# Kernel tuning notes

Hardware: AMD Instinct MI355X
Metric: run time of the kernel (lower is better)

## Reference

```python
import jax, jax.numpy as jnp
import numpy as np

EMBED = 1024
HEADS = 16
HEAD_DIM = EMBED // HEADS
LN_EPS = 1e-5


def _layer_norm(x, g, b):
    m = jnp.mean(x, axis=-1, keepdims=True)
    v = jnp.mean((x - m) ** 2, axis=-1, keepdims=True)
    return (x - m) / jnp.sqrt(v + LN_EPS) * g + b


def _rope(x):
    # x: (b, H, n, D); standard rotary: freqs repeated (cat(freqs, freqs)), rotate_half
    D = x.shape[-1]
    n = x.shape[2]
    inv_freq = 1.0 / (10000.0 ** (jnp.arange(0, D, 2, dtype=jnp.float32) / D))
    freqs = jnp.arange(n, dtype=jnp.float32)[:, None] * inv_freq[None, :]  # (n, D/2)
    emb = jnp.concatenate([freqs, freqs], axis=-1)  # (n, D)
    cos, sin = jnp.cos(emb), jnp.sin(emb)
    rot = jnp.concatenate([-x[..., D // 2:], x[..., : D // 2]], axis=-1)
    return x * cos + rot * sin


def setup_inputs() -> dict:
    key = jax.random.key(0)
    ks = jax.random.split(key, 8)
    E = EMBED
    s_in = 1.0 / np.sqrt(E)
    return {
        "x": jax.random.normal(ks[0], (2, 2048, E), dtype=jnp.float32),
        "in_proj_w": jax.random.uniform(ks[1], (3 * E, E), jnp.float32, -s_in, s_in),
        "in_proj_b": jnp.zeros((3 * E,), jnp.float32),
        "out_proj_w": jax.random.uniform(ks[2], (E, E), jnp.float32, -s_in, s_in),
        "out_proj_b": jnp.zeros((E,), jnp.float32),
        "geglu_w": jax.random.uniform(ks[3], (2 * E, E), jnp.float32, -s_in, s_in),
        "geglu_b": jnp.zeros((2 * E,), jnp.float32),
        "ln1_g": jnp.ones((E,), jnp.float32),
        "ln1_b": jnp.zeros((E,), jnp.float32),
        "ln2_g": jnp.ones((E,), jnp.float32),
        "ln2_b": jnp.zeros((E,), jnp.float32),
    }


def reference(x, in_proj_w, in_proj_b, out_proj_w, out_proj_b,
              geglu_w, geglu_b, ln1_g, ln1_b, ln2_g, ln2_b):
    b, n, E = x.shape
    H, D = HEADS, HEAD_DIM

    # RoPE applied to raw x (q = k = v = x in the module)
    xh = x.reshape(b, n, H, D).transpose(0, 2, 1, 3)  # (b,H,n,D)
    qr = _rope(xh)
    kr = qr  # q and k are identical pre-projection
    q = qr.transpose(0, 2, 1, 3).reshape(b, n, E)
    k = kr.transpose(0, 2, 1, 3).reshape(b, n, E)
    v = x

    # MultiheadAttention (batch-first semantics): in-proj, per-head SDPA, out-proj
    w_q, w_k, w_v = jnp.split(in_proj_w, 3, axis=0)
    b_q, b_k, b_v = jnp.split(in_proj_b, 3, axis=0)
    qp = (q @ w_q.T + b_q).reshape(b, n, H, D).transpose(0, 2, 1, 3)
    kp = (k @ w_k.T + b_k).reshape(b, n, H, D).transpose(0, 2, 1, 3)
    vp = (v @ w_v.T + b_v).reshape(b, n, H, D).transpose(0, 2, 1, 3)
    scores = jnp.einsum("bhqd,bhkd->bhqk", qp, kp) / jnp.sqrt(jnp.float32(D))
    attn = jax.nn.softmax(scores, axis=-1)
    ctx = jnp.einsum("bhqk,bhkd->bhqd", attn, vp)
    ctx = ctx.transpose(0, 2, 1, 3).reshape(b, n, E)
    attn_out = ctx @ out_proj_w.T + out_proj_b

    # residual + LN1
    h = _layer_norm(x + attn_out, ln1_g, ln1_b)

    # GeGLU: Linear(E -> 2E), chunk, value * gelu(gate) (exact erf gelu like torch)
    proj = h @ geglu_w.T + geglu_b
    val, gate = jnp.split(proj, 2, axis=-1)
    fc_out = val * jax.nn.gelu(gate, approximate=False)

    # residual + LN2
    return _layer_norm(h + fc_out, ln2_g, ln2_b)
```

## Files before the change

kernel.cpp:

```cpp
#include <hip/hip_runtime.h>


typedef __bf16 bf16;
typedef bf16 bf16x8 __attribute__((ext_vector_type(8)));
typedef bf16 bf16x4 __attribute__((ext_vector_type(4)));
typedef float f32x4 __attribute__((ext_vector_type(4)));
typedef float f32x16 __attribute__((ext_vector_type(16)));

#define EMB 1024
#define SEQ 2048
#define NTOK 4096
#define NH 16
#define HD 64

__device__ __forceinline__ f32x4 mfma16(bf16x8 a, bf16x8 b, f32x4 c) {
  return __builtin_amdgcn_mfma_f32_16x16x32_bf16(a, b, c, 0, 0, 0);
}
__device__ __forceinline__ f32x16 mfma32(bf16x8 a, bf16x8 b, f32x16 c) {
  return __builtin_amdgcn_mfma_f32_32x32x16_bf16(a, b, c, 0, 0, 0);
}

__device__ __forceinline__ void gll16(const void* g, void* l) {
  __builtin_amdgcn_global_load_lds(
      (const __attribute__((address_space(1))) void*)g,
      (__attribute__((address_space(3))) void*)l, 16, 0, 0);
}

__device__ __forceinline__ unsigned pk2(float a, float b) {
  union { bf16 h[2]; unsigned u; } t;
  t.h[0] = (bf16)a; t.h[1] = (bf16)b;
  return t.u;
}


__global__ __launch_bounds__(256) void rope_cast(
    const float* __restrict__ x, bf16* __restrict__ xb, bf16* __restrict__ qr) {
  int idx = blockIdx.x * 256 + threadIdx.x;
  int row = idx >> 9;
  int i = idx & 511;
  int h = i >> 5, d2 = i & 31;
  int pos = row & (SEQ - 1);
  int c0 = h * HD + d2;
  size_t base = (size_t)row * EMB;
  float x0 = x[base + c0], x1 = x[base + c0 + 32];
  float invf = exp2f(-(float)d2 * 0.4152410118609203f);
  float ang = (float)pos * invf;
  float sn, cs;
  sincosf(ang, &sn, &cs);
  qr[base + c0] = (bf16)(x0 * cs - x1 * sn);
  qr[base + c0 + 32] = (bf16)(x1 * cs + x0 * sn);
  xb[base + c0] = (bf16)x0;
  xb[base + c0 + 32] = (bf16)x1;
}

__global__ __launch_bounds__(256) void cast_w(
    const float* __restrict__ w, bf16* __restrict__ o, int n) {
  int i = (blockIdx.x * 256 + threadIdx.x) * 4;
  if (i < n) {
    float4 f = *(const float4*)(w + i);
    o[i] = (bf16)f.x; o[i + 1] = (bf16)f.y;
    o[i + 2] = (bf16)f.z; o[i + 3] = (bf16)f.w;
  }
}

__global__ __launch_bounds__(256) void gemm_in(
    const bf16* __restrict__ Aq, const bf16* __restrict__ Ax,
    const bf16* __restrict__ W, const float* __restrict__ bias,
    bf16* __restrict__ qk, bf16* __restrict__ vT) {
  __shared__ bf16 As[128 * 32];
  __shared__ bf16 Bs[128 * 32];
  const int tid = threadIdx.x, lane = tid & 63, wave = tid >> 6;
  const int quad = lane >> 4, l16 = lane & 15;
  const int m0 = blockIdx.y * 128, n0 = blockIdx.x * 128;
  const bf16* A = (n0 < 2048) ? Aq : Ax;
  const int K = 1024;
  const int wm = (wave >> 1) * 64, wn = (wave & 1) * 64;
  const int srow = wave * 32 + (lane >> 2);
  const int scol = (lane & 3) * 8;
  f32x4 acc[4][4] = {};
  for (int k0 = 0; k0 < K; k0 += 32) {
    __syncthreads();
    gll16(A + (size_t)(m0 + srow) * K + k0 + scol, As + wave * 1024);
    gll16(A + (size_t)(m0 + srow + 16) * K + k0 + scol, As + wave * 1024 + 512);
    gll16(W + (size_t)(n0 + srow) * K + k0 + scol, Bs + wave * 1024);
    gll16(W + (size_t)(n0 + srow + 16) * K + k0 + scol, Bs + wave * 1024 + 512);
    __syncthreads();
    bf16x8 af[4], bw[4];
#pragma unroll
    for (int t = 0; t < 4; ++t) {
      af[t] = *(const bf16x8*)(As + (wm + t * 16 + l16) * 32 + quad * 8);
      bw[t] = *(const bf16x8*)(Bs + (wn + t * 16 + l16) * 32 + quad * 8);
    }
#pragma unroll
    for (int mt = 0; mt < 4; ++mt)
#pragma unroll
      for (int nt = 0; nt < 4; ++nt)
        acc[mt][nt] = mfma16(af[mt], bw[nt], acc[mt][nt]);
  }
  if (n0 < 2048) {
#pragma unroll
    for (int mt = 0; mt < 4; ++mt)
      for (int nt = 0; nt < 4; ++nt) {
        const int n = n0 + wn + nt * 16 + l16;
        const float bv = bias[n];
#pragma unroll
        for (int r = 0; r < 4; ++r) {
          const int m = m0 + wm + mt * 16 + quad * 4 + r;
          qk[(size_t)m * 2048 + n] = (bf16)(acc[mt][nt][r] + bv);
        }
      }
  } else {
#pragma unroll
    for (int mt = 0; mt < 4; ++mt)
      for (int nt = 0; nt < 4; ++nt) {
        const int n = n0 + wn + nt * 16 + l16;
        const float bv = bias[n];
        const int m = m0 + wm + mt * 16 + quad * 4;
        const int bb = m >> 11, s = m & 2047;
        bf16x4 pkv;
#pragma unroll
        for (int r = 0; r < 4; ++r) pkv[r] = (bf16)(acc[mt][nt][r] + bv);
        *(bf16x4*)(vT + (((size_t)bb * 1024 + (n - 2048)) << 11) + s) = pkv;
      }
  }
}

__global__ __launch_bounds__(256) void gemm_bt(
    const bf16* __restrict__ A, const bf16* __restrict__ W,
    const float* __restrict__ bias,
    float* __restrict__ outF, bf16* __restrict__ outB,
    int M, int N, int K) {
  __shared__ bf16 As[128 * 32];
  __shared__ bf16 Bs[128 * 32];
  const int tid = threadIdx.x, lane = tid & 63, wave = tid >> 6;
  const int quad = lane >> 4, l16 = lane & 15;
  const int m0 = blockIdx.y * 128, n0 = blockIdx.x * 128;
  const int wm = (wave >> 1) * 64, wn = (wave & 1) * 64;
  const int srow = wave * 32 + (lane >> 2);
  const int scol = (lane & 3) * 8;
  f32x4 acc[4][4] = {};
  for (int k0 = 0; k0 < K; k0 += 32) {
    __syncthreads();
    gll16(A + (size_t)(m0 + srow) * K + k0 + scol, As + wave * 1024);
    gll16(A + (size_t)(m0 + srow + 16) * K + k0 + scol, As + wave * 1024 + 512);
    gll16(W + (size_t)(n0 + srow) * K + k0 + scol, Bs + wave * 1024);
    gll16(W + (size_t)(n0 + srow + 16) * K + k0 + scol, Bs + wave * 1024 + 512);
    __syncthreads();
    bf16x8 af[4], bw[4];
#pragma unroll
    for (int t = 0; t < 4; ++t) {
      af[t] = *(const bf16x8*)(As + (wm + t * 16 + l16) * 32 + quad * 8);
      bw[t] = *(const bf16x8*)(Bs + (wn + t * 16 + l16) * 32 + quad * 8);
    }
#pragma unroll
    for (int mt = 0; mt < 4; ++mt)
#pragma unroll
      for (int nt = 0; nt < 4; ++nt)
        acc[mt][nt] = mfma16(af[mt], bw[nt], acc[mt][nt]);
  }
#pragma unroll
  for (int mt = 0; mt < 4; ++mt)
    for (int nt = 0; nt < 4; ++nt) {
      const int n = n0 + wn + nt * 16 + l16;
      const float bv = bias ? bias[n] : 0.0f;
#pragma unroll
      for (int r = 0; r < 4; ++r) {
        const int m = m0 + wm + mt * 16 + quad * 4 + r;
        const float v = acc[mt][nt][r] + bv;
        if (outF) outF[(size_t)m * N + n] = v;
        if (outB) outB[(size_t)m * N + n] = (bf16)v;
      }
    }
}

__global__ __launch_bounds__(256) void gemm_bt64(
    const bf16* __restrict__ A, const bf16* __restrict__ W,
    const float* __restrict__ bias, float* __restrict__ outF,
    int M, int N, int K) {
  __shared__ bf16 As[128 * 32];
  __shared__ bf16 Bs[64 * 32];
  const int tid = threadIdx.x, lane = tid & 63, wave = tid >> 6;
  const int quad = lane >> 4, l16 = lane & 15;
  const int m0 = blockIdx.y * 128, n0 = blockIdx.x * 64;
  const int wm = (wave >> 1) * 64, wn = (wave & 1) * 32;
  const int srow = wave * 32 + (lane >> 2);
  const int srowB = wave * 16 + (lane >> 2);
  const int scol = (lane & 3) * 8;
  f32x4 acc[4][2] = {};
  for (int k0 = 0; k0 < K; k0 += 32) {
    __syncthreads();
    gll16(A + (size_t)(m0 + srow) * K + k0 + scol, As + wave * 1024);
    gll16(A + (size_t)(m0 + srow + 16) * K + k0 + scol, As + wave * 1024 + 512);
    gll16(W + (size_t)(n0 + srowB) * K + k0 + scol, Bs + wave * 512);
    __syncthreads();
    bf16x8 af[4], bw[2];
#pragma unroll
    for (int t = 0; t < 4; ++t)
      af[t] = *(const bf16x8*)(As + (wm + t * 16 + l16) * 32 + quad * 8);
#pragma unroll
    for (int t = 0; t < 2; ++t)
      bw[t] = *(const bf16x8*)(Bs + (wn + t * 16 + l16) * 32 + quad * 8);
#pragma unroll
    for (int mt = 0; mt < 4; ++mt)
#pragma unroll
      for (int nt = 0; nt < 2; ++nt)
        acc[mt][nt] = mfma16(af[mt], bw[nt], acc[mt][nt]);
  }
#pragma unroll
  for (int mt = 0; mt < 4; ++mt)
    for (int nt = 0; nt < 2; ++nt) {
      const int n = n0 + wn + nt * 16 + l16;
      const float bv = bias[n];
#pragma unroll
      for (int r = 0; r < 4; ++r) {
        const int m = m0 + wm + mt * 16 + quad * 4 + r;
        outF[(size_t)m * N + n] = acc[mt][nt][r] + bv;
      }
    }
}

__global__ __launch_bounds__(256) void attn9(
    const bf16* __restrict__ QK, const bf16* __restrict__ VT,
    bf16* __restrict__ ctx) {
  __shared__ __align__(16) bf16 Ks[2][8192];
  __shared__ __align__(16) bf16 Vs[2][8192];
  __shared__ float Linv[4][32];
  const int tid = threadIdx.x, lane = tid & 63, wave = tid >> 6;
  const int hi = lane >> 5, l31 = lane & 31, l7 = lane & 7;
  const int bid = blockIdx.x;
  const int hb = (bid & 7) * 4 + ((bid >> 3) & 3);
  const int qt = bid >> 5;
  const int h = hb & 15, b = hb >> 4;

  bf16x8 qf[4];
  {
    const int qrow = qt * 128 + wave * 32 + l31;
    const bf16* qp = QK + (size_t)(b * SEQ + qrow) * 2048 + h * HD + hi * 8;
#pragma unroll
    for (int t = 0; t < 4; ++t) {
      bf16x8 v = *(const bf16x8*)(qp + t * 16);
#pragma unroll
      for (int j = 0; j < 8; ++j) v[j] = (bf16)((float)v[j] * 0.125f);
      qf[t] = v;
    }
  }
  f32x16 o0 = {}, o1 = {};
  float lpart = 0.0f;

  const int krow0 = tid >> 3;
  const int ksc = tid & 7;
  const int vrow0 = tid >> 4;
  const int vc16 = tid & 15;
  const int og = (vc16 >> 1) * 16 + (vc16 & 1) * 4;
  const bf16* kg = QK + (size_t)(b * SEQ) * 2048 + 1024 + h * HD + ksc * 8;
  const bf16* vg = VT + ((size_t)(b * NH + h) * HD) * 2048;

  bf16x8 kcur[4];
  uint2 va[4], vb[4];
#pragma unroll
  for (int p = 0; p < 4; ++p) {
    kcur[p] = *(const bf16x8*)(kg + (size_t)(krow0 + p * 32) * 2048);
    va[p] = *(const uint2*)(vg + (size_t)(vrow0 + p * 16) * 2048 + og);
    vb[p] = *(const uint2*)(vg + (size_t)(vrow0 + p * 16) * 2048 + og + 8);
  }
#pragma unroll
  for (int p = 0; p < 4; ++p) {
    const int kr = krow0 + p * 32;
    *(bf16x8*)(Ks[0] + kr * 64 + ((ksc ^ (kr & 7)) * 8)) = kcur[p];
    const int vr = vrow0 + p * 16;
    union { uint2 u2[2]; bf16x8 v; } vv;
    vv.u2[0] = va[p]; vv.u2[1] = vb[p];
    *(bf16x8*)(Vs[0] + vr * 128 + ((vc16 ^ (vr & 7)) * 8)) = vv.v;
  }
#pragma unroll
  for (int p = 0; p < 4; ++p) {
    kcur[p] = *(const bf16x8*)(kg + (size_t)(128 + krow0 + p * 32) * 2048);
    va[p] = *(const uint2*)(vg + (size_t)(vrow0 + p * 16) * 2048 + 128 + og);
    vb[p] = *(const uint2*)(vg + (size_t)(vrow0 + p * 16) * 2048 + 128 + og + 8);
  }

  for (int t = 0; t < 16; ++t) {
    __syncthreads();
    const bf16* ks = Ks[t & 1];
    const bf16* vs = Vs[t & 1];
    if (t + 1 < 16) {
      bf16* kd = Ks[(t + 1) & 1];
      bf16* vd = Vs[(t + 1) & 1];
#pragma unroll
      for (int p = 0; p < 4; ++p) {
        const int kr = krow0 + p * 32;
        *(bf16x8*)(kd + kr * 64 + ((ksc ^ (kr & 7)) * 8)) = kcur[p];
        const int vr = vrow0 + p * 16;
        union { uint2 u2[2]; bf16x8 v; } vv;
        vv.u2[0] = va[p]; vv.u2[1] = vb[p];
        *(bf16x8*)(vd + vr * 128 + ((vc16 ^ (vr & 7)) * 8)) = vv.v;
      }
      if (t + 2 < 16) {
        const int kb2 = (t + 2) * 128;
#pragma unroll
        for (int p = 0; p < 4; ++p) {
          kcur[p] = *(const bf16x8*)(kg + (size_t)(kb2 + krow0 + p * 32) * 2048);
          va[p] = *(const uint2*)(vg + (size_t)(vrow0 + p * 16) * 2048 + kb2 + og);
          vb[p] = *(const uint2*)(vg + (size_t)(vrow0 + p * 16) * 2048 + kb2 + og + 8);
        }
      }
    }
#pragma unroll
    for (int half = 0; half < 2; ++half) {
      const bf16* ksh = ks + half * 64 * 64;
      f32x16 s0 = {}, s1 = {};
#pragma unroll
      for (int tt = 0; tt < 4; ++tt) {
        const int swc = ((tt * 2 + hi) ^ l7) * 8;
        bf16x8 k0 = *(const bf16x8*)(ksh + l31 * 64 + swc);
        bf16x8 k1 = *(const bf16x8*)(ksh + (32 + l31) * 64 + swc);
        s0 = mfma32(k0, qf[tt], s0);
        s1 = mfma32(k1, qf[tt], s1);
      }
      unsigned u[16];
#pragma unroll
      for (int g = 0; g < 8; ++g) {
        const int base = (g & 3) * 4;
        float e0, e1, e2, e3;
        if (g < 4) {
          e0 = __expf(s0[base]); e1 = __expf(s0[base + 1]);
          e2 = __expf(s0[base + 2]); e3 = __expf(s0[base + 3]);
        } else {
          e0 = __expf(s1[base]); e1 = __expf(s1[base + 1]);
          e2 = __expf(s1[base + 2]); e3 = __expf(s1[base + 3]);
        }
        lpart += (e0 + e1) + (e2 + e3);
        u[g * 2] = pk2(e0, e1);
        u[g * 2 + 1] = pk2(e2, e3);
      }
#pragma unroll
      for (int kk = 0; kk < 4; ++kk) {
        union { unsigned w[4]; bf16x8 v; } fw;
        fw.w[0] = u[4 * kk]; fw.w[1] = u[4 * kk + 1];
        fw.w[2] = u[4 * kk + 2]; fw.w[3] = u[4 * kk + 3];
        const int c16 = (8 * half + 2 * kk + hi) ^ l7;
        bf16x8 v0 = *(const bf16x8*)(vs + l31 * 128 + c16 * 8);
        bf16x8 v1 = *(const bf16x8*)(vs + (32 + l31) * 128 + c16 * 8);
        o0 = mfma32(fw.v, v0, o0);
        o1 = mfma32(fw.v, v1, o1);
      }
    }
  }
  float ltot = lpart + __shfl_xor(lpart, 32, 64);
  if (lane < 32) Linv[wave][lane] = 1.0f / ltot;
#pragma unroll
  for (int r = 0; r < 16; ++r) {
    const int qloc = (r & 3) + 8 * (r >> 2) + 4 * hi;
    const float inv = Linv[wave][qloc];
    const int qrow = qt * 128 + wave * 32 + qloc;
    bf16* cp = ctx + (size_t)(b * SEQ + qrow) * EMB + h * HD;
    cp[l31] = (bf16)(o0[r] * inv);
    cp[32 + l31] = (bf16)(o1[r] * inv);
  }
}

__global__ __launch_bounds__(256) void ln1_k(
    const float* __restrict__ x, const float* __restrict__ ao,
    const float* __restrict__ g, const float* __restrict__ bta,
    float* __restrict__ hF, bf16* __restrict__ hB) {
  int row = blockIdx.x, tid = threadIdx.x;
  const float* xr = x + (size_t)row * EMB;
  const float* ar = ao + (size_t)row * EMB;
  float v[4], s = 0.0f, s2 = 0.0f;
#pragma unroll
  for (int i = 0; i < 4; ++i) {
    float t = xr[tid + i * 256] + ar[tid + i * 256];
    v[i] = t; s += t; s2 += t * t;
  }
#pragma unroll
  for (int off = 1; off < 64; off <<= 1) {
    s += __shfl_xor(s, off, 64);
    s2 += __shfl_xor(s2, off, 64);
  }
  __shared__ float red[8];
  int wave = tid >> 6, lane = tid & 63;
  if (lane == 0) { red[wave] = s; red[4 + wave] = s2; }
  __syncthreads();
  s = red[0] + red[1] + red[2] + red[3];
  s2 = red[4] + red[5] + red[6] + red[7];
  float mean = s * (1.0f / EMB);
  float var = s2 * (1.0f / EMB) - mean * mean;
  float inv = rsqrtf(var + 1e-5f);
#pragma unroll
  for (int i = 0; i < 4; ++i) {
    int c = tid + i * 256;
    float t = (v[i] - mean) * inv * g[c] + bta[c];
    hF[(size_t)row * EMB + c] = t;
    hB[(size_t)row * EMB + c] = (bf16)t;
  }
}

__global__ __launch_bounds__(256) void geglu_ln2(
    const float* __restrict__ h, const bf16* __restrict__ proj,
    const float* __restrict__ g, const float* __restrict__ bta,
    float* __restrict__ out) {
  int row = blockIdx.x, tid = threadIdx.x;
  const float* hr = h + (size_t)row * EMB;
  const bf16* pr = proj + (size_t)row * 2048;
  float v[4], s = 0.0f, s2 = 0.0f;
#pragma unroll
  for (int i = 0; i < 4; ++i) {
    int c = tid + i * 256;
    float val = (float)pr[c];
    float gate = (float)pr[1024 + c];
    float ge = 0.5f * gate * (1.0f + erff(gate * 0.70710678f));
    float t = hr[c] + val * ge;
    v[i] = t; s += t; s2 += t * t;
  }
#pragma unroll
  for (int off = 1; off < 64; off <<= 1) {
    s += __shfl_xor(s, off, 64);
    s2 += __shfl_xor(s2, off, 64);
  }
  __shared__ float red[8];
  int wave = tid >> 6, lane = tid & 63;
  if (lane == 0) { red[wave] = s; red[4 + wave] = s2; }
  __syncthreads();
  s = red[0] + red[1] + red[2] + red[3];
  s2 = red[4] + red[5] + red[6] + red[7];
  float mean = s * (1.0f / EMB);
  float var = s2 * (1.0f / EMB) - mean * mean;
  float inv = rsqrtf(var + 1e-5f);
#pragma unroll
  for (int i = 0; i < 4; ++i) {
    int c = tid + i * 256;
    out[(size_t)row * EMB + c] = (v[i] - mean) * inv * g[c] + bta[c];
  }
}

extern "C" void kernel_launch(void* const* d_in, const int* in_sizes, int n_in,
                              void* d_out, int out_size, void* d_ws, size_t ws_size,
                              hipStream_t stream) {
  const float* x = (const float*)d_in[0];
  const float* inW = (const float*)d_in[1];
  const float* inB = (const float*)d_in[2];
  const float* outW = (const float*)d_in[3];
  const float* opB = (const float*)d_in[4];
  const float* ggW = (const float*)d_in[5];
  const float* ggB = (const float*)d_in[6];
  const float* g1 = (const float*)d_in[7];
  const float* b1 = (const float*)d_in[8];
  const float* g2 = (const float*)d_in[9];
  const float* b2 = (const float*)d_in[10];
  float* out = (float*)d_out;
  char* ws = (char*)d_ws;
  const size_t MB = 1ull << 20;
  bf16* xb = (bf16*)(ws);
  bf16* qr = (bf16*)(ws + 8 * MB);
  bf16* ctx = (bf16*)(ws + 8 * MB);
  bf16* wI = (bf16*)(ws + 16 * MB);
  bf16* wO = (bf16*)(ws + 22 * MB);
  bf16* wG = (bf16*)(ws + 24 * MB);
  bf16* qk = (bf16*)(ws + 28 * MB);
  bf16* projB = (bf16*)(ws + 28 * MB);
  bf16* vbT = (bf16*)(ws + 44 * MB);
  float* ao = (float*)(ws + 44 * MB);
  bf16* hB = (bf16*)(ws + 60 * MB);

  rope_cast<<<NTOK * 512 / 256, 256, 0, stream>>>(x, xb, qr);
  cast_w<<<(3072 * 1024 / 4) / 256, 256, 0, stream>>>(inW, wI, 3072 * 1024);
  cast_w<<<(1024 * 1024 / 4) / 256, 256, 0, stream>>>(outW, wO, 1024 * 1024);
  cast_w<<<(2048 * 1024 / 4) / 256, 256, 0, stream>>>(ggW, wG, 2048 * 1024);
  gemm_in<<<dim3(24, 32), 256, 0, stream>>>(qr, xb, wI, inB, qk, vbT);
  attn9<<<512, 256, 0, stream>>>(qk, vbT, ctx);
  gemm_bt64<<<dim3(16, 32), 256, 0, stream>>>(ctx, wO, opB, ao,
                                              NTOK, 1024, 1024);
  ln1_k<<<NTOK, 256, 0, stream>>>(x, ao, g1, b1, ao, hB);
  gemm_bt<<<dim3(16, 32), 256, 0, stream>>>(hB, wG, ggB, nullptr, projB,
                                            NTOK, 2048, 1024);
  geglu_ln2<<<NTOK, 256, 0, stream>>>(ao, projB, g2, b2, out);
}
```

Baseline: 273.2 us.

## Pre-swizzle K/V tiles in projection epilogue and stream them via direct LDS loads

The in-projection epilogue now writes K and V directly in the per-tile swizzled LDS layout the attention kernel expects. It also folds the 1/sqrt(D) scale into Q and log2(e) into K. The attention kernel then copies each contiguous 32KB tile into LDS with global_load_lds instead of loading through registers and storing with swizzle. It uses exp2 in place of expf and computes the softmax row sums with an extra MFMA against a ones vector, removing the shuffle and LDS reduction. The risks are scattered, uncoalesced 2-byte stores in the K epilogue and an extra MFMA per PV step.

```diff
diff --git a/kernel.cpp b/kernel.cpp
--- a/kernel.cpp
+++ b/kernel.cpp
@@ -66,7 +66,7 @@
 __global__ __launch_bounds__(256) void gemm_in(
     const bf16* __restrict__ Aq, const bf16* __restrict__ Ax,
     const bf16* __restrict__ W, const float* __restrict__ bias,
-    bf16* __restrict__ qk, bf16* __restrict__ vT) {
+    bf16* __restrict__ qb, bf16* __restrict__ kv) {
   __shared__ bf16 As[128 * 32];
   __shared__ bf16 Bs[128 * 32];
   const int tid = threadIdx.x, lane = tid & 63, wave = tid >> 6;
@@ -97,7 +97,7 @@
       for (int nt = 0; nt < 4; ++nt)
         acc[mt][nt] = mfma16(af[mt], bw[nt], acc[mt][nt]);
   }
-  if (n0 < 2048) {
+  if (n0 < 1024) {
 #pragma unroll
     for (int mt = 0; mt < 4; ++mt)
       for (int nt = 0; nt < 4; ++nt) {
@@ -106,21 +106,45 @@
 #pragma unroll
         for (int r = 0; r < 4; ++r) {
           const int m = m0 + wm + mt * 16 + quad * 4 + r;
-          qk[(size_t)m * 2048 + n] = (bf16)(acc[mt][nt][r] + bv);
+          qb[(size_t)m * 1024 + n] = (bf16)((acc[mt][nt][r] + bv) * 0.125f);
         }
       }
-  } else {
+  } else if (n0 < 2048) {
 #pragma unroll
     for (int mt = 0; mt < 4; ++mt)
       for (int nt = 0; nt < 4; ++nt) {
         const int n = n0 + wn + nt * 16 + l16;
         const float bv = bias[n];
+        const int kd = n - 1024, hh = kd >> 6, d = kd & 63;
+        const int dc = d >> 3, dl = d & 7;
+#pragma unroll
+        for (int r = 0; r < 4; ++r) {
+          const int m = m0 + wm + mt * 16 + quad * 4 + r;
+          const int bb = m >> 11, s = m & 2047;
+          const int t = s >> 7, kr = s & 127;
+          const size_t base = ((size_t)((bb * 16 + hh) * 16 + t)) * 16384;
+          kv[base + kr * 64 + ((dc ^ (kr & 7)) << 3) + dl] =
+              (bf16)((acc[mt][nt][r] + bv) * 1.4426950408889634f);
+        }
+      }
+  } else {
+#pragma unroll
+    for (int mt = 0; mt < 4; ++mt)
+      for (int nt = 0; nt < 4; ++nt) {
+        const int n = n0 + wn + nt * 16 + l16;
+        const float bv = bias[n];
+        const int vd = n - 2048, hh = vd >> 6, d = vd & 63;
         const int m = m0 + wm + mt * 16 + quad * 4;
         const int bb = m >> 11, s = m & 2047;
+        const int t = s >> 7, kt = s & 127;
+        const int g = kt >> 4, w = kt & 15;
+        const int c = 2 * g + ((w >> 2) & 1);
+        const int slot = (w & 8) ? 4 : 0;
+        const size_t base = ((size_t)((bb * 16 + hh) * 16 + t)) * 16384 + 8192;
         bf16x4 pkv;
 #pragma unroll
         for (int r = 0; r < 4; ++r) pkv[r] = (bf16)(acc[mt][nt][r] + bv);
-        *(bf16x4*)(vT + (((size_t)bb * 1024 + (n - 2048)) << 11) + s) = pkv;
+        *(bf16x4*)(kv + base + d * 128 + ((c ^ (d & 7)) << 3) + slot) = pkv;
       }
   }
 }
@@ -219,12 +243,10 @@
     }
 }
 
-__global__ __launch_bounds__(256) void attn9(
-    const bf16* __restrict__ QK, const bf16* __restrict__ VT,
+__global__ __launch_bounds__(256) void attn10(
+    const bf16* __restrict__ Q, const bf16* __restrict__ KV,
     bf16* __restrict__ ctx) {
-  __shared__ __align__(16) bf16 Ks[2][8192];
-  __shared__ __align__(16) bf16 Vs[2][8192];
-  __shared__ float Linv[4][32];
+  __shared__ __align__(16) bf16 kvb[2][16384];
   const int tid = threadIdx.x, lane = tid & 63, wave = tid >> 6;
   const int hi = lane >> 5, l31 = lane & 31, l7 = lane & 7;
   const int bid = blockIdx.x;
@@ -235,82 +257,47 @@
   bf16x8 qf[4];
   {
     const int qrow = qt * 128 + wave * 32 + l31;
-    const bf16* qp = QK + (size_t)(b * SEQ + qrow) * 2048 + h * HD + hi * 8;
-#pragma unroll
-    for (int t = 0; t < 4; ++t) {
-      bf16x8 v = *(const bf16x8*)(qp + t * 16);
-#pragma unroll
-      for (int j = 0; j < 8; ++j) v[j] = (bf16)((float)v[j] * 0.125f);
-      qf[t] = v;
-    }
-  }
-  f32x16 o0 = {}, o1 = {};
-  float lpart = 0.0f;
-
-  const int krow0 = tid >> 3;
-  const int ksc = tid & 7;
-  const int vrow0 = tid >> 4;
-  const int vc16 = tid & 15;
-  const int og = (vc16 >> 1) * 16 + (vc16 & 1) * 4;
-  const bf16* kg = QK + (size_t)(b * SEQ) * 2048 + 1024 + h * HD + ksc * 8;
-  const bf16* vg = VT + ((size_t)(b * NH + h) * HD) * 2048;
-
-  bf16x8 kcur[4];
-  uint2 va[4], vb[4];
-#pragma unroll
-  for (int p = 0; p < 4; ++p) {
-    kcur[p] = *(const bf16x8*)(kg + (size_t)(krow0 + p * 32) * 2048);
-    va[p] = *(const uint2*)(vg + (size_t)(vrow0 + p * 16) * 2048 + og);
-    vb[p] = *(const uint2*)(vg + (size_t)(vrow0 + p * 16) * 2048 + og + 8);
-  }
-#pragma unroll
-  for (int p = 0; p < 4; ++p) {
-    const int kr = krow0 + p * 32;
-    *(bf16x8*)(Ks[0] + kr * 64 + ((ksc ^ (kr & 7)) * 8)) = kcur[p];
-    const int vr = vrow0 + p * 16;
-    union { uint2 u2[2]; bf16x8 v; } vv;
-    vv.u2[0] = va[p]; vv.u2[1] = vb[p];
-    *(bf16x8*)(Vs[0] + vr * 128 + ((vc16 ^ (vr & 7)) * 8)) = vv.v;
-  }
-#pragma unroll
-  for (int p = 0; p < 4; ++p) {
-    kcur[p] = *(const bf16x8*)(kg + (size_t)(128 + krow0 + p * 32) * 2048);
-    va[p] = *(const uint2*)(vg + (size_t)(vrow0 + p * 16) * 2048 + 128 + og);
-    vb[p] = *(const uint2*)(vg + (size_t)(vrow0 + p * 16) * 2048 + 128 + og + 8);
-  }
+    const bf16* qp = Q + (size_t)(b * SEQ + qrow) * 1024 + h * HD + hi * 8;
+#pragma unroll
+    for (int t = 0; t < 4; ++t) qf[t] = *(const bf16x8*)(qp + t * 16);
+  }
+  const bf16* kvg = KV + ((size_t)(b * NH + h) * 16) * 16384 + wave * 2048 + lane * 8;
+#pragma unroll
+  for (int i = 0; i < 4; ++i) {
+    gll16(kvg + i * 512, kvb[0] + wave * 2048 + i * 512);
+    gll16(kvg + 8192 + i * 512, kvb[0] + 8192 + wave * 2048 + i * 512);
+  }
+  f32x16 o0 = {}, o1 = {}, lacc = {};
+  const f32x16 zf = {};
+  const bf16 onec = (bf16)1.0f;
+  const bf16x8 onef = {onec, onec, onec, onec, onec, onec, onec, onec};
 
   for (int t = 0; t < 16; ++t) {
     __syncthreads();
-    const bf16* ks = Ks[t & 1];
-    const bf16* vs = Vs[t & 1];
     if (t + 1 < 16) {
-      bf16* kd = Ks[(t + 1) & 1];
-      bf16* vd = Vs[(t + 1) & 1];
-#pragma unroll
-      for (int p = 0; p < 4; ++p) {
-        const int kr = krow0 + p * 32;
-        *(bf16x8*)(kd + kr * 64 + ((ksc ^ (kr & 7)) * 8)) = kcur[p];
-        const int vr = vrow0 + p * 16;
-        union { uint2 u2[2]; bf16x8 v; } vv;
-        vv.u2[0] = va[p]; vv.u2[1] = vb[p];
-        *(bf16x8*)(vd + vr * 128 + ((vc16 ^ (vr & 7)) * 8)) = vv.v;
-      }
-      if (t + 2 < 16) {
-        const int kb2 = (t + 2) * 128;
-#pragma unroll
-        for (int p = 0; p < 4; ++p) {
-          kcur[p] = *(const bf16x8*)(kg + (size_t)(kb2 + krow0 + p * 32) * 2048);
-          va[p] = *(const uint2*)(vg + (size_t)(vrow0 + p * 16) * 2048 + kb2 + og);
-          vb[p] = *(const uint2*)(vg + (size_t)(vrow0 + p * 16) * 2048 + kb2 + og + 8);
-        }
-      }
-    }
+      const bf16* src = kvg + (size_t)(t + 1) * 16384;
+      bf16* dst = kvb[(t + 1) & 1] + wave * 2048;
+#pragma unroll
+      for (int i = 0; i < 4; ++i) {
+        gll16(src + i * 512, dst + i * 512);
+        gll16(src + 8192 + i * 512, dst + 8192 + i * 512);
+      }
+    }
+    const bf16* ks = kvb[t & 1];
+    const bf16* vs = kvb[t & 1] + 8192;
 #pragma unroll
     for (int half = 0; half < 2; ++half) {
-      const bf16* ksh = ks + half * 64 * 64;
-      f32x16 s0 = {}, s1 = {};
-#pragma unroll
-      for (int tt = 0; tt < 4; ++tt) {
+      const bf16* ksh = ks + half * 4096;
+      f32x16 s0, s1;
+      {
+        const int swc = (hi ^ l7) * 8;
+        bf16x8 k0 = *(const bf16x8*)(ksh + l31 * 64 + swc);
+        bf16x8 k1 = *(const bf16x8*)(ksh + (32 + l31) * 64 + swc);
+        s0 = mfma32(k0, qf[0], zf);
+        s1 = mfma32(k1, qf[0], zf);
+      }
+#pragma unroll
+      for (int tt = 1; tt < 4; ++tt) {
         const int swc = ((tt * 2 + hi) ^ l7) * 8;
         bf16x8 k0 = *(const bf16x8*)(ksh + l31 * 64 + swc);
         bf16x8 k1 = *(const bf16x8*)(ksh + (32 + l31) * 64 + swc);
@@ -323,13 +310,16 @@
         const int base = (g & 3) * 4;
         float e0, e1, e2, e3;
         if (g < 4) {
-          e0 = __expf(s0[base]); e1 = __expf(s0[base + 1]);
-          e2 = __expf(s0[base + 2]); e3 = __expf(s0[base + 3]);
+          e0 = __builtin_amdgcn_exp2f(s0[base]);
+          e1 = __builtin_amdgcn_exp2f(s0[base + 1]);
+          e2 = __builtin_amdgcn_exp2f(s0[base + 2]);
+          e3 = __builtin_amdgcn_exp2f(s0[base + 3]);
         } else {
-          e0 = __expf(s1[base]); e1 = __expf(s1[base + 1]);
-          e2 = __expf(s1[base + 2]); e3 = __expf(s1[base + 3]);
+          e0 = __builtin_amdgcn_exp2f(s1[base]);
+          e1 = __builtin_amdgcn_exp2f(s1[base + 1]);
+          e2 = __builtin_amdgcn_exp2f(s1[base + 2]);
+          e3 = __builtin_amdgcn_exp2f(s1[base + 3]);
         }
-        lpart += (e0 + e1) + (e2 + e3);
         u[g * 2] = pk2(e0, e1);
         u[g * 2 + 1] = pk2(e2, e3);
       }
@@ -341,17 +331,16 @@
         const int c16 = (8 * half + 2 * kk + hi) ^ l7;
         bf16x8 v0 = *(const bf16x8*)(vs + l31 * 128 + c16 * 8);
         bf16x8 v1 = *(const bf16x8*)(vs + (32 + l31) * 128 + c16 * 8);
+        lacc = mfma32(fw.v, onef, lacc);
         o0 = mfma32(fw.v, v0, o0);
         o1 = mfma32(fw.v, v1, o1);
       }
     }
   }
-  float ltot = lpart + __shfl_xor(lpart, 32, 64);
-  if (lane < 32) Linv[wave][lane] = 1.0f / ltot;
 #pragma unroll
   for (int r = 0; r < 16; ++r) {
     const int qloc = (r & 3) + 8 * (r >> 2) + 4 * hi;
-    const float inv = Linv[wave][qloc];
+    const float inv = 1.0f / lacc[r];
     const int qrow = qt * 128 + wave * 32 + qloc;
     bf16* cp = ctx + (size_t)(b * SEQ + qrow) * EMB + h * HD;
     cp[l31] = (bf16)(o0[r] * inv);
@@ -451,23 +440,23 @@
   char* ws = (char*)d_ws;
   const size_t MB = 1ull << 20;
   bf16* xb = (bf16*)(ws);
+  bf16* hB = (bf16*)(ws);
   bf16* qr = (bf16*)(ws + 8 * MB);
   bf16* ctx = (bf16*)(ws + 8 * MB);
   bf16* wI = (bf16*)(ws + 16 * MB);
   bf16* wO = (bf16*)(ws + 22 * MB);
   bf16* wG = (bf16*)(ws + 24 * MB);
-  bf16* qk = (bf16*)(ws + 28 * MB);
+  bf16* qb = (bf16*)(ws + 28 * MB);
+  bf16* kv = (bf16*)(ws + 36 * MB);
   bf16* projB = (bf16*)(ws + 28 * MB);
-  bf16* vbT = (bf16*)(ws + 44 * MB);
-  float* ao = (float*)(ws + 44 * MB);
-  bf16* hB = (bf16*)(ws + 60 * MB);
+  float* ao = (float*)(ws + 52 * MB);
 
   rope_cast<<<NTOK * 512 / 256, 256, 0, stream>>>(x, xb, qr);
   cast_w<<<(3072 * 1024 / 4) / 256, 256, 0, stream>>>(inW, wI, 3072 * 1024);
   cast_w<<<(1024 * 1024 / 4) / 256, 256, 0, stream>>>(outW, wO, 1024 * 1024);
   cast_w<<<(2048 * 1024 / 4) / 256, 256, 0, stream>>>(ggW, wG, 2048 * 1024);
-  gemm_in<<<dim3(24, 32), 256, 0, stream>>>(qr, xb, wI, inB, qk, vbT);
-  attn9<<<512, 256, 0, stream>>>(qk, vbT, ctx);
+  gemm_in<<<dim3(24, 32), 256, 0, stream>>>(qr, xb, wI, inB, qb, kv);
+  attn10<<<512, 256, 0, stream>>>(qb, kv, ctx);
   gemm_bt64<<<dim3(16, 32), 256, 0, stream>>>(ctx, wO, opB, ao,
                                               NTOK, 1024, 1024);
   ln1_k<<<NTOK, 256, 0, stream>>>(x, ao, g1, b1, ao, hB);
```

Measured after the change: 278.9 us. 2.1% more time.
